# Performance work log

Measured on AMD Instinct MI355X. Metric: run time of the kernel, lower is better.

The kernel has to match this reference:

```python
import jax, jax.numpy as jnp
import numpy as np

STATE_DIM = 67  # latent_dim 64 + (x, y, yaw)
IU0, IU1 = np.triu_indices(STATE_DIM)  # row-major i<=j, matches nested loop order
DT = 0.1


def _conv_relu(x, w, b):
    # x: (B, Cin, L), w: (Cout, Cin, 5), stride 2, pad 2 -> (B, Cout, ceil(L/2))
    y = jax.lax.conv_general_dilated(x, w, window_strides=(2,), padding=[(2, 2)],
                                     dimension_numbers=('NCH', 'OIH', 'NCH'))
    return jax.nn.relu(y + b[None, :, None])


def setup_inputs() -> dict:
    key = jax.random.key(0)
    ks = jax.random.split(key, 13)
    B = 32768
    s = 0.05
    return {
        'lidar_in': jax.random.normal(ks[0], (B, 360), jnp.float32),
        'odom_in': jax.random.normal(ks[1], (B, 3), jnp.float32),
        'conv1_w': jax.random.normal(ks[2], (16, 1, 5), jnp.float32) * s,
        'conv1_b': jax.random.normal(ks[3], (16,), jnp.float32) * s,
        'conv2_w': jax.random.normal(ks[4], (32, 16, 5), jnp.float32) * s,
        'conv2_b': jax.random.normal(ks[5], (32,), jnp.float32) * s,
        'conv3_w': jax.random.normal(ks[6], (64, 32, 5), jnp.float32) * s,
        'conv3_b': jax.random.normal(ks[7], (64,), jnp.float32) * s,
        'fc_w': jax.random.normal(ks[8], (64, 64 * 45), jnp.float32) * 0.01,
        'fc_b': jax.random.normal(ks[9], (64,), jnp.float32) * s,
        'sindy_w': jax.random.normal(ks[10], (3, 2480), jnp.float32) * 0.01,
    }


def reference(lidar_in, odom_in, conv1_w, conv1_b, conv2_w, conv2_b,
              conv3_w, conv3_b, fc_w, fc_b, sindy_w):
    B = lidar_in.shape[0]
    # --- LiDAR feature extractor ---
    x = lidar_in[:, None, :]                       # (B, 1, 360)
    x = _conv_relu(x, conv1_w, conv1_b)            # (B, 16, 180)
    x = _conv_relu(x, conv2_w, conv2_b)            # (B, 32, 90)
    x = _conv_relu(x, conv3_w, conv3_b)            # (B, 64, 45)
    x = x.reshape(B, -1)                           # (B, 2880)
    z = x @ fc_w.T + fc_b                          # (B, 64)
    # --- state and SINDy library ---
    state = jnp.concatenate([z, odom_in], axis=1)  # (B, 67)
    quad = state[:, IU0] * state[:, IU1]           # (B, 2278) triangular products
    library = jnp.concatenate([
        jnp.ones((B, 1), state.dtype), state, quad,
        jnp.sin(state), jnp.cos(state)], axis=1)   # (B, 2480)
    dxyz = library @ sindy_w.T                     # (B, 3)
    return odom_in + DT * dxyz                     # (x,y,yaw)_next
```

## Files before the change

### kernel.cpp

```cpp
#include <hip/hip_runtime.h>
#include <hip/hip_bf16.h>

typedef __attribute__((ext_vector_type(8))) short bf16x8;
typedef __attribute__((ext_vector_type(4))) short short4v;
typedef __attribute__((ext_vector_type(4))) float f32x4;
typedef __attribute__((ext_vector_type(4))) float float4v;
typedef __attribute__((ext_vector_type(4))) int int4v;

constexpr int L0 = 360, L2n = 90, L3n = 45;
constexpr int SD = 67, NQ = 2278, LIB = 2480, FCIN = 2880;
constexpr int C1_CH = 20, S1B = 186 * C1_CH * 2;
constexpr int C2_CH = 44, S2B = 96 * C2_CH * 2;
constexpr int S3E = 2888;
constexpr int XB_STRIDE = 392;

constexpr int A_C3 = 0;
constexpr int A_C3SZ = 8 * S3E * 2;
constexpr int A_C1 = A_C3 + A_C3SZ;
constexpr int A_C1SZ = 2 * S1B;
constexpr int A_C2 = A_C1 + A_C1SZ;
constexpr int A_C2SZ = 2 * S2B + 512;
constexpr int A_XB = A_C2 + A_C2SZ;
constexpr int A_XBSZ = 2 * XB_STRIDE * 2;
constexpr int A_PAR = A_XB + A_XBSZ;
constexpr int A_SMEM = A_PAR + 448;
static_assert(A_SMEM <= 81920, "A LDS over 2-block budget");

constexpr int B_ST = 0;
constexpr int B_STSZ = 64 * 68 * 4;
constexpr int B_SB = B_ST + B_STSZ;
constexpr int B_SBSZ = 64 * 104 * 2;
constexpr int B_YB = B_SB + B_SBSZ;
constexpr int B_YBSZ = 3 * 64 * 84 * 2;
constexpr int B_SMEM = B_YB + B_YBSZ;
static_assert(B_SMEM <= 81920, "B LDS over 2-block budget");

constexpr size_t WSO_FCW = 0;
constexpr size_t WSO_W2F = WSO_FCW + 64 * FCIN * 2;
constexpr size_t WSO_W3F = WSO_W2F + 3 * 32 * 32 * 2;
constexpr size_t WSO_UB  = WSO_W3F + 5 * 64 * 32 * 2;
constexpr size_t WSO_W1F = WSO_UB + 3 * 80 * 96 * 2;
constexpr size_t WS_WEIGHTS = WSO_W1F + 16 * 32 * 2;
constexpr size_t WSO_C3 = WS_WEIGHTS;

__device__ __forceinline__ short f2b(float f) {
    return (short)__builtin_bit_cast(unsigned short, __float2bfloat16(f));
}
__device__ __forceinline__ float b2f(short s) {
    unsigned int u = ((unsigned int)(unsigned short)s) << 16;
    return __builtin_bit_cast(float, u);
}
__device__ __forceinline__ bf16x8 ld_frag8(const char* p) {
    union { bf16x8 v; short4v h[2]; } u;
    u.h[0] = *(const short4v*)(p);
    u.h[1] = *(const short4v*)(p + 8);
    return u.v;
}

__global__ __launch_bounds__(256) void pre_convert(
    const float* __restrict__ fcw, const float* __restrict__ w2,
    const float* __restrict__ w3, const float* __restrict__ w1,
    const float* __restrict__ sw, char* __restrict__ ws) {
    int idx = blockIdx.x * 256 + threadIdx.x;
    if (idx < 64 * FCIN) {
        int j = idx / FCIN, mp = idx % FCIN;
        int o = mp & 63, t = mp >> 6;
        ((short*)(ws + WSO_FCW))[idx] = f2b(fcw[j * FCIN + o * 45 + t]);
    }
    if (idx < 3 * 32 * 32) {
        int p = idx >> 10, o = (idx >> 5) & 31, k32 = idx & 31;
        int kk = 2 * p + (k32 >> 4), ic = k32 & 15;
        float v = (kk < 5) ? w2[(o * 16 + ic) * 5 + kk] : 0.f;
        ((short*)(ws + WSO_W2F))[idx] = f2b(v);
    }
    if (idx < 5 * 64 * 32) {
        int kk = idx >> 11, o = (idx >> 5) & 63, ic = idx & 31;
        ((short*)(ws + WSO_W3F))[idx] = f2b(w3[(o * 32 + ic) * 5 + kk]);
    }
    if (idx < 3 * 80 * 96) {
        int r = idx / (80 * 96), rem = idx % (80 * 96), nn = rem / 96, kk = rem % 96;
        float v = 0.f;
        if (nn < 68 && kk < 68) {
            if (nn == 67 && kk == 67) v = sw[r * LIB];
            else if (nn == 67) v = 0.5f * sw[r * LIB + 1 + kk];
            else if (kk == 67) v = 0.5f * sw[r * LIB + 1 + nn];
            else {
                int a = nn < kk ? nn : kk, b = nn < kk ? kk : nn;
                int q = a * 67 - (a * (a - 1)) / 2 + (b - a);
                v = sw[r * LIB + 68 + q];
                if (nn != kk) v *= 0.5f;
            }
        }
        ((short*)(ws + WSO_UB))[idx] = f2b(v);
    }
    if (idx < 512) {
        int o = idx >> 5, k = idx & 31;
        ((short*)(ws + WSO_W1F))[idx] = (k < 5) ? f2b(w1[o * 5 + k]) : (short)0;
    }
}

__global__ __launch_bounds__(512, 2) void conv_pipe(
    const float* __restrict__ lidar, const float* __restrict__ b1,
    const float* __restrict__ b2, const float* __restrict__ b3,
    char* __restrict__ ws)
{
    __shared__ char smem[A_SMEM];
    const int tid = threadIdx.x;
    const int wv = tid >> 6, lane = tid & 63;
    const int lr = lane & 15, lg = lane >> 4;
    const long blk = blockIdx.x;
    float* par = (float*)(smem + A_PAR);
    short* xb = (short*)(smem + A_XB);

    const int sW = wv & 1;
    const int qW = wv >> 1;
    const int o0_2 = (qW >> 1) * 16;
    const int o0_3 = qW * 16;

    bf16x8 af1 = *(const bf16x8*)(ws + WSO_W1F + (lr * 32 + lg * 8) * 2);
    bf16x8 af2[3], af3[5];
    #pragma unroll
    for (int p = 0; p < 3; p++)
        af2[p] = *(const bf16x8*)(ws + WSO_W2F + ((p * 32 + o0_2 + lr) * 32 + lg * 8) * 2);
    #pragma unroll
    for (int kk = 0; kk < 5; kk++)
        af3[kk] = *(const bf16x8*)(ws + WSO_W3F + ((kk * 64 + o0_3 + lr) * 32 + lg * 8) * 2);

    auto stage_xb = [&](int g) {
        float4v v = ((const float4v*)(lidar + (blk * 8 + g * 2) * L0))[tid];
        int si = tid / 90, c = tid % 90;
        short* dst = xb + si * XB_STRIDE + 2 + 4 * c;
        *(int*)(dst) = (int)(unsigned short)f2b(v[0]) | ((int)(unsigned short)f2b(v[1]) << 16);
        *(int*)(dst + 2) = (int)(unsigned short)f2b(v[2]) | ((int)(unsigned short)f2b(v[3]) << 16);
    };

    if (tid < 16) par[tid] = b1[tid];
    else if (tid < 48) par[16 + tid - 16] = b2[tid - 16];
    else if (tid < 112) par[48 + tid - 48] = b3[tid - 48];
    if (tid >= 120 && tid < 124) {
        int s = (tid - 120) >> 1, h = (tid - 120) & 1;
        ((int*)xb)[s * (XB_STRIDE / 2) + (h ? 181 : 0)] = 0;
    }
    if (tid >= 128 && tid < 208) {
        int i = tid - 128, slot = i / 40, r = i % 40;
        const int rows[4] = {2, 3, 184, 185};
        *(int*)(smem + A_C1 + slot * S1B + rows[r / 10] * (C1_CH * 2) + (r % 10) * 4) = 0;
    }
    if (tid >= 208 && tid < 384) {
        int i = tid - 208, slot = i / 88, r = i % 88;
        const int rows[4] = {2, 3, 94, 95};
        *(int*)(smem + A_C2 + slot * S2B + rows[r / 22] * (C2_CH * 2) + (r % 22) * 4) = 0;
    }
    if (tid < 180) stage_xb(0);
    __syncthreads();

    float bia1_[4], bia2_[4], bia3_[4];
    #pragma unroll
    for (int r = 0; r < 4; r++) {
        bia1_[r] = par[lg * 4 + r];
        bia2_[r] = par[16 + o0_2 + lg * 4 + r];
        bia3_[r] = par[48 + o0_3 + lg * 4 + r];
    }

    auto conv1_body = [&]() {
        const short* xs = xb + sW * XB_STRIDE;
        char* c1s = smem + A_C1 + sW * S1B;
        #pragma unroll
        for (int i = 0; i < 3; ++i) {
            const int t = (qW * 3 + i) * 16 + lr;
            bf16x8 bv = {0, 0, 0, 0, 0, 0, 0, 0};
            if (lg == 0) {
                const short* xp = xs + 2 * t;
                int d0 = *(const int*)(xp);
                int d1 = *(const int*)(xp + 2);
                bv[0] = (short)(d0 & 0xffff); bv[1] = (short)(d0 >> 16);
                bv[2] = (short)(d1 & 0xffff); bv[3] = (short)(d1 >> 16);
                bv[4] = xp[4];
            }
            f32x4 acc = {0.f, 0.f, 0.f, 0.f};
            acc = __builtin_amdgcn_mfma_f32_16x16x32_bf16(af1, bv, acc, 0, 0, 0);
            if (t < 180) {
                short4v pk = { f2b(fmaxf(acc[0] + bia1_[0], 0.f)), f2b(fmaxf(acc[1] + bia1_[1], 0.f)),
                               f2b(fmaxf(acc[2] + bia1_[2], 0.f)), f2b(fmaxf(acc[3] + bia1_[3], 0.f)) };
                *(short4v*)(c1s + (t + 4) * (C1_CH * 2) + lg * 8) = pk;
            }
        }
    };

    conv1_body();
    __syncthreads();

    for (int g = 0; g < 4; ++g) {
        {
            const int orow = o0_2 + lg * 4;
            const int kkp = lane >> 5, i0 = (lg & 1) * 8;
            const char* bp = smem + A_C1 + sW * S1B
                           + (2 * lr + kkp + 2) * (C1_CH * 2) + i0 * 2
                           + (qW & 1) * 3840;
            char* c2s = smem + A_C2 + sW * S2B;
            const bool stg = (g < 3) && (tid < 180);
            float4v lv;
            if (stg) lv = ((const float4v*)(lidar + (blk * 8 + (g + 1) * 2) * L0))[tid];
            #pragma unroll
            for (int i = 0; i < 3; ++i) {
                f32x4 acc = {0.f, 0.f, 0.f, 0.f};
                #pragma unroll
                for (int p = 0; p < 3; p++) {
                    bf16x8 bf = ld_frag8(bp + i * 1280 + p * 80);
                    acc = __builtin_amdgcn_mfma_f32_16x16x32_bf16(af2[p], bf, acc, 0, 0, 0);
                }
                const int tw = ((qW & 1) * 3 + i) * 16 + lr;
                if (tw < L2n) {
                    short4v pk = { f2b(fmaxf(acc[0] + bia2_[0], 0.f)), f2b(fmaxf(acc[1] + bia2_[1], 0.f)),
                                   f2b(fmaxf(acc[2] + bia2_[2], 0.f)), f2b(fmaxf(acc[3] + bia2_[3], 0.f)) };
                    *(short4v*)(c2s + (tw + 4) * (C2_CH * 2) + orow * 2) = pk;
                }
            }
            if (stg) {
                int si = tid / 90, c = tid % 90;
                short* dst = xb + si * XB_STRIDE + 2 + 4 * c;
                *(int*)(dst) = (int)(unsigned short)f2b(lv[0]) | ((int)(unsigned short)f2b(lv[1]) << 16);
                *(int*)(dst + 2) = (int)(unsigned short)f2b(lv[2]) | ((int)(unsigned short)f2b(lv[3]) << 16);
            }
        }
        __syncthreads();

        {
            const int orow = o0_3 + lg * 4;
            const char* bp2 = smem + A_C2 + sW * S2B
                            + (2 * lr + 2) * (C2_CH * 2) + lg * 16;
            char* c3s = smem + A_C3 + (g * 2 + sW) * (S3E * 2);
            #pragma unroll
            for (int tt = 0; tt < 3; ++tt) {
                f32x4 acc = {0.f, 0.f, 0.f, 0.f};
                #pragma unroll
                for (int kk = 0; kk < 5; kk++) {
                    bf16x8 bf = ld_frag8(bp2 + tt * 2816 + kk * 88);
                    acc = __builtin_amdgcn_mfma_f32_16x16x32_bf16(af3[kk], bf, acc, 0, 0, 0);
                }
                const int tw = tt * 16 + lr;
                if (tw < L3n) {
                    short4v pk = { f2b(fmaxf(acc[0] + bia3_[0], 0.f)), f2b(fmaxf(acc[1] + bia3_[1], 0.f)),
                                   f2b(fmaxf(acc[2] + bia3_[2], 0.f)), f2b(fmaxf(acc[3] + bia3_[3], 0.f)) };
                    int byteoff = (tw * 64 + orow) * 2;
                    byteoff ^= (tw & 7) << 4;
                    *(short4v*)(c3s + byteoff) = pk;
                }
            }
            if (g < 3) conv1_body();
        }
        __syncthreads();
    }

    for (int i4 = tid; i4 < 8 * 361; i4 += 512) {
        int k8 = i4 >> 3, sample = i4 & 7;
        int wb = k8 * 16;
        int src = wb ^ (((k8 >> 3) & 7) << 4);
        int4v v = *(const int4v*)(smem + A_C3 + sample * (S3E * 2) + src);
        ((int4v*)(ws + WSO_C3))[(blk * 361 + k8) * 8 + sample] = v;
    }
}

__global__ __launch_bounds__(512, 2) void fc_tail(
    const float* __restrict__ odom, const float* __restrict__ fcb,
    const float* __restrict__ sw, const char* __restrict__ ws,
    float* __restrict__ out)
{
    __shared__ char smem[B_SMEM];
    const int tid = threadIdx.x;
    const int wv = tid >> 6, lane = tid & 63;
    const int lr = lane & 15, lg = lane >> 4;
    const long blk = blockIdx.x;
    const long sbase = blk * 64;
    const short* c3g = (const short*)(ws + WSO_C3);
    const short* fcwb = (const short*)(ws + WSO_FCW);
    float* st = (float*)(smem + B_ST);
    short* sb = (short*)(smem + B_SB);
    short* yb = (short*)(smem + B_YB);

    {
        const int jt = wv & 3, mh = wv >> 2, j0 = jt * 16;
        const float fj = fcb[j0 + lr];
        const short* brow = fcwb + (long)(j0 + lr) * FCIN + lg * 8;
        const int sb0 = mh * 32;
        const long n0 = sbase + sb0 + lr;
        const long n1 = n0 + 16;
        const short* ar0 = c3g + ((n0 >> 3) * 361 + lg) * 64 + (n0 & 7) * 8;
        const short* ar1 = c3g + ((n1 >> 3) * 361 + lg) * 64 + (n1 & 7) * 8;
        f32x4 acc0 = {0.f, 0.f, 0.f, 0.f}, acc1 = {0.f, 0.f, 0.f, 0.f};
        bf16x8 a0 = *(const bf16x8*)(ar0);
        bf16x8 a1 = *(const bf16x8*)(ar1);
        bf16x8 b0 = *(const bf16x8*)(brow);
        for (int kt = 0; kt < 90; ++kt) {
            bf16x8 ac0 = a0, ac1 = a1, bc = b0;
            if (kt < 89) {
                a0 = *(const bf16x8*)(ar0 + (kt + 1) * 256);
                a1 = *(const bf16x8*)(ar1 + (kt + 1) * 256);
                b0 = *(const bf16x8*)(brow + (kt + 1) * 32);
            }
            acc0 = __builtin_amdgcn_mfma_f32_16x16x32_bf16(ac0, bc, acc0, 0, 0, 0);
            acc1 = __builtin_amdgcn_mfma_f32_16x16x32_bf16(ac1, bc, acc1, 0, 0, 0);
        }
        #pragma unroll
        for (int r = 0; r < 4; ++r) {
            st[(sb0 + lg * 4 + r) * 68 + j0 + lr] = acc0[r] + fj;
            st[(sb0 + 16 + lg * 4 + r) * 68 + j0 + lr] = acc1[r] + fj;
        }
    }
    __syncthreads();

    for (int i = tid; i < 64 * 104; i += 512) {
        int sr = i / 104, c = i % 104;
        short v;
        if (c < 64) v = f2b(st[sr * 68 + c]);
        else if (c < 67) v = f2b(odom[(sbase + sr) * 3 + (c - 64)]);
        else if (c == 67) v = (short)0x3F80;
        else v = 0;
        sb[i] = v;
    }
    __syncthreads();

    {
        const short* ubb = (const short*)(ws + WSO_UB);
        for (int job = wv; job < 15; job += 8) {
            const int r = job / 5, nt = job % 5;
            const short* ub = ubb + (r * 80 + nt * 16 + lr) * 96 + lg * 8;
            #pragma unroll
            for (int mt = 0; mt < 4; ++mt) {
                f32x4 acc = {0.f, 0.f, 0.f, 0.f};
                #pragma unroll
                for (int kt = 0; kt < 3; ++kt) {
                    bf16x8 av = *(const bf16x8*)(sb + (mt * 16 + lr) * 104 + kt * 32 + lg * 8);
                    bf16x8 bv = *(const bf16x8*)(ub + kt * 32);
                    acc = __builtin_amdgcn_mfma_f32_16x16x32_bf16(av, bv, acc, 0, 0, 0);
                }
                #pragma unroll
                for (int rr = 0; rr < 4; ++rr)
                    yb[(r * 64 + mt * 16 + lg * 4 + rr) * 84 + nt * 16 + lr] = f2b(acc[rr]);
            }
        }
    }
    __syncthreads();

    for (int ss = 0; ss < 8; ++ss) {
        const int sr = wv * 8 + ss;
        const long n = sbase + sr;
        float sv = st[sr * 68 + lane];
        float sn = __sinf(sv), cs = __cosf(sv);
        float d0 = sw[2346 + lane] * sn + sw[2413 + lane] * cs
                 + b2f(yb[(0 * 64 + sr) * 84 + lane]) * sv;
        float d1 = sw[LIB + 2346 + lane] * sn + sw[LIB + 2413 + lane] * cs
                 + b2f(yb[(1 * 64 + sr) * 84 + lane]) * sv;
        float d2 = sw[2 * LIB + 2346 + lane] * sn + sw[2 * LIB + 2413 + lane] * cs
                 + b2f(yb[(2 * 64 + sr) * 84 + lane]) * sv;
        if (lane < 3) {
            float ov = odom[n * 3 + lane];
            float sn2 = __sinf(ov), cs2 = __cosf(ov);
            int j2 = 64 + lane;
            d0 += sw[2346 + j2] * sn2 + sw[2413 + j2] * cs2 + b2f(yb[(0 * 64 + sr) * 84 + j2]) * ov;
            d1 += sw[LIB + 2346 + j2] * sn2 + sw[LIB + 2413 + j2] * cs2 + b2f(yb[(1 * 64 + sr) * 84 + j2]) * ov;
            d2 += sw[2 * LIB + 2346 + j2] * sn2 + sw[2 * LIB + 2413 + j2] * cs2 + b2f(yb[(2 * 64 + sr) * 84 + j2]) * ov;
        } else if (lane == 3) {
            d0 += b2f(yb[(0 * 64 + sr) * 84 + 67]);
            d1 += b2f(yb[(1 * 64 + sr) * 84 + 67]);
            d2 += b2f(yb[(2 * 64 + sr) * 84 + 67]);
        }
        #pragma unroll
        for (int off = 32; off; off >>= 1) {
            d0 += __shfl_xor(d0, off, 64);
            d1 += __shfl_xor(d1, off, 64);
            d2 += __shfl_xor(d2, off, 64);
        }
        if (lane == 0) {
            out[n * 3 + 0] = odom[n * 3 + 0] + 0.1f * d0;
            out[n * 3 + 1] = odom[n * 3 + 1] + 0.1f * d1;
            out[n * 3 + 2] = odom[n * 3 + 2] + 0.1f * d2;
        }
    }
}

extern "C" void kernel_launch(void* const* d_in, const int* in_sizes, int n_in,
                              void* d_out, int out_size, void* d_ws, size_t ws_size,
                              hipStream_t stream) {
    const float* lidar = (const float*)d_in[0];
    const float* odom  = (const float*)d_in[1];
    const float* w1    = (const float*)d_in[2];
    const float* b1    = (const float*)d_in[3];
    const float* w2    = (const float*)d_in[4];
    const float* b2    = (const float*)d_in[5];
    const float* w3    = (const float*)d_in[6];
    const float* b3    = (const float*)d_in[7];
    const float* fcw   = (const float*)d_in[8];
    const float* fcb   = (const float*)d_in[9];
    const float* sw    = (const float*)d_in[10];
    float* out = (float*)d_out;

    int B = in_sizes[0] / L0;
    size_t ws_total = WSO_C3 + (size_t)B * S3E * 2;
    if (ws_size < ws_total) return;

    char* ws = (char*)d_ws;
    pre_convert<<<(64 * FCIN + 255) / 256, 256, 0, stream>>>(fcw, w2, w3, w1, sw, ws);
    conv_pipe<<<B / 8, 512, 0, stream>>>(lidar, b1, b2, b3, ws);
    fc_tail<<<B / 64, 512, 0, stream>>>(odom, fcb, sw, ws, out);
}
```

Measured before the change: 194.7 us.

## Reuse conv2/conv3 B fragments across two output-channel tiles per wave

Conv2 and conv3 work is re-split so each wave computes two 16-channel output tiles sharing one loaded LDS B fragment, instead of one channel tile over three time tiles. This halves LDS fragment loads per MFMA and gives two independent accumulator chains. The time tiles are now split unevenly across waves (some waves do 2 tiles, others 1), which creates load imbalance. Holding twice as many weight fragments in registers also raises register pressure under the 512x2 launch bound.

```diff
diff --git a/kernel.cpp b/kernel.cpp
--- a/kernel.cpp
+++ b/kernel.cpp
@@ -114,17 +114,21 @@
 
     const int sW = wv & 1;
     const int qW = wv >> 1;
-    const int o0_2 = (qW >> 1) * 16;
-    const int o0_3 = qW * 16;
+    const int op3 = qW & 1;
+    const int th3 = qW >> 1;
 
     bf16x8 af1 = *(const bf16x8*)(ws + WSO_W1F + (lr * 32 + lg * 8) * 2);
-    bf16x8 af2[3], af3[5];
+    bf16x8 af2[2][3], af3[2][5];
     #pragma unroll
-    for (int p = 0; p < 3; p++)
-        af2[p] = *(const bf16x8*)(ws + WSO_W2F + ((p * 32 + o0_2 + lr) * 32 + lg * 8) * 2);
+    for (int ot = 0; ot < 2; ot++)
+        #pragma unroll
+        for (int p = 0; p < 3; p++)
+            af2[ot][p] = *(const bf16x8*)(ws + WSO_W2F + ((p * 32 + ot * 16 + lr) * 32 + lg * 8) * 2);
     #pragma unroll
-    for (int kk = 0; kk < 5; kk++)
-        af3[kk] = *(const bf16x8*)(ws + WSO_W3F + ((kk * 64 + o0_3 + lr) * 32 + lg * 8) * 2);
+    for (int j = 0; j < 2; j++)
+        #pragma unroll
+        for (int kk = 0; kk < 5; kk++)
+            af3[j][kk] = *(const bf16x8*)(ws + WSO_W3F + ((kk * 64 + (op3 * 2 + j) * 16 + lr) * 32 + lg * 8) * 2);
 
     auto stage_xb = [&](int g) {
         float4v v = ((const float4v*)(lidar + (blk * 8 + g * 2) * L0))[tid];
@@ -154,12 +158,14 @@
     if (tid < 180) stage_xb(0);
     __syncthreads();
 
-    float bia1_[4], bia2_[4], bia3_[4];
+    float bia1_[4], bia2_[2][4], bia3_[2][4];
     #pragma unroll
     for (int r = 0; r < 4; r++) {
         bia1_[r] = par[lg * 4 + r];
-        bia2_[r] = par[16 + o0_2 + lg * 4 + r];
-        bia3_[r] = par[48 + o0_3 + lg * 4 + r];
+        #pragma unroll
+        for (int ot = 0; ot < 2; ot++) bia2_[ot][r] = par[16 + ot * 16 + lg * 4 + r];
+        #pragma unroll
+        for (int j = 0; j < 2; j++) bia3_[j][r] = par[48 + (op3 * 2 + j) * 16 + lg * 4 + r];
     }
 
     auto conv1_body = [&]() {
@@ -192,28 +198,34 @@
 
     for (int g = 0; g < 4; ++g) {
         {
-            const int orow = o0_2 + lg * 4;
             const int kkp = lane >> 5, i0 = (lg & 1) * 8;
             const char* bp = smem + A_C1 + sW * S1B
-                           + (2 * lr + kkp + 2) * (C1_CH * 2) + i0 * 2
-                           + (qW & 1) * 3840;
+                           + (2 * lr + kkp + 2) * (C1_CH * 2) + i0 * 2;
             char* c2s = smem + A_C2 + sW * S2B;
             const bool stg = (g < 3) && (tid < 180);
             float4v lv;
             if (stg) lv = ((const float4v*)(lidar + (blk * 8 + (g + 1) * 2) * L0))[tid];
-            #pragma unroll
-            for (int i = 0; i < 3; ++i) {
-                f32x4 acc = {0.f, 0.f, 0.f, 0.f};
+
+            const int tbase = (qW < 2) ? qW * 2 : (2 + qW);
+            const int nT = (qW < 2) ? 2 : 1;
+            for (int it = 0; it < nT; ++it) {
+                const int T = tbase + it;
+                f32x4 a0 = {0.f, 0.f, 0.f, 0.f}, a1 = {0.f, 0.f, 0.f, 0.f};
                 #pragma unroll
                 for (int p = 0; p < 3; p++) {
-                    bf16x8 bf = ld_frag8(bp + i * 1280 + p * 80);
-                    acc = __builtin_amdgcn_mfma_f32_16x16x32_bf16(af2[p], bf, acc, 0, 0, 0);
+                    bf16x8 bf = ld_frag8(bp + T * 1280 + p * 80);
+                    a0 = __builtin_amdgcn_mfma_f32_16x16x32_bf16(af2[0][p], bf, a0, 0, 0, 0);
+                    a1 = __builtin_amdgcn_mfma_f32_16x16x32_bf16(af2[1][p], bf, a1, 0, 0, 0);
                 }
-                const int tw = ((qW & 1) * 3 + i) * 16 + lr;
+                const int tw = T * 16 + lr;
                 if (tw < L2n) {
-                    short4v pk = { f2b(fmaxf(acc[0] + bia2_[0], 0.f)), f2b(fmaxf(acc[1] + bia2_[1], 0.f)),
-                                   f2b(fmaxf(acc[2] + bia2_[2], 0.f)), f2b(fmaxf(acc[3] + bia2_[3], 0.f)) };
-                    *(short4v*)(c2s + (tw + 4) * (C2_CH * 2) + orow * 2) = pk;
+                    short4v pk0 = { f2b(fmaxf(a0[0] + bia2_[0][0], 0.f)), f2b(fmaxf(a0[1] + bia2_[0][1], 0.f)),
+                                    f2b(fmaxf(a0[2] + bia2_[0][2], 0.f)), f2b(fmaxf(a0[3] + bia2_[0][3], 0.f)) };
+                    short4v pk1 = { f2b(fmaxf(a1[0] + bia2_[1][0], 0.f)), f2b(fmaxf(a1[1] + bia2_[1][1], 0.f)),
+                                    f2b(fmaxf(a1[2] + bia2_[1][2], 0.f)), f2b(fmaxf(a1[3] + bia2_[1][3], 0.f)) };
+                    char* wp = c2s + (tw + 4) * (C2_CH * 2);
+                    *(short4v*)(wp + lg * 8) = pk0;
+                    *(short4v*)(wp + 32 + lg * 8) = pk1;
                 }
             }
             if (stg) {
@@ -226,25 +238,32 @@
         __syncthreads();
 
         {
-            const int orow = o0_3 + lg * 4;
             const char* bp2 = smem + A_C2 + sW * S2B
                             + (2 * lr + 2) * (C2_CH * 2) + lg * 16;
             char* c3s = smem + A_C3 + (g * 2 + sW) * (S3E * 2);
-            #pragma unroll
-            for (int tt = 0; tt < 3; ++tt) {
-                f32x4 acc = {0.f, 0.f, 0.f, 0.f};
+            const int ttbase = (th3 == 0) ? 0 : 2;
+            const int nT3 = (th3 == 0) ? 2 : 1;
+            for (int it = 0; it < nT3; ++it) {
+                const int tt = ttbase + it;
+                f32x4 a0 = {0.f, 0.f, 0.f, 0.f}, a1 = {0.f, 0.f, 0.f, 0.f};
                 #pragma unroll
                 for (int kk = 0; kk < 5; kk++) {
                     bf16x8 bf = ld_frag8(bp2 + tt * 2816 + kk * 88);
-                    acc = __builtin_amdgcn_mfma_f32_16x16x32_bf16(af3[kk], bf, acc, 0, 0, 0);
+                    a0 = __builtin_amdgcn_mfma_f32_16x16x32_bf16(af3[0][kk], bf, a0, 0, 0, 0);
+                    a1 = __builtin_amdgcn_mfma_f32_16x16x32_bf16(af3[1][kk], bf, a1, 0, 0, 0);
                 }
                 const int tw = tt * 16 + lr;
                 if (tw < L3n) {
-                    short4v pk = { f2b(fmaxf(acc[0] + bia3_[0], 0.f)), f2b(fmaxf(acc[1] + bia3_[1], 0.f)),
-                                   f2b(fmaxf(acc[2] + bia3_[2], 0.f)), f2b(fmaxf(acc[3] + bia3_[3], 0.f)) };
-                    int byteoff = (tw * 64 + orow) * 2;
-                    byteoff ^= (tw & 7) << 4;
-                    *(short4v*)(c3s + byteoff) = pk;
+                    short4v pk0 = { f2b(fmaxf(a0[0] + bia3_[0][0], 0.f)), f2b(fmaxf(a0[1] + bia3_[0][1], 0.f)),
+                                    f2b(fmaxf(a0[2] + bia3_[0][2], 0.f)), f2b(fmaxf(a0[3] + bia3_[0][3], 0.f)) };
+                    short4v pk1 = { f2b(fmaxf(a1[0] + bia3_[1][0], 0.f)), f2b(fmaxf(a1[1] + bia3_[1][1], 0.f)),
+                                    f2b(fmaxf(a1[2] + bia3_[1][2], 0.f)), f2b(fmaxf(a1[3] + bia3_[1][3], 0.f)) };
+                    const int orow0 = op3 * 32 + lg * 4;
+                    const int orow1 = op3 * 32 + 16 + lg * 4;
+                    int bo0 = ((tw * 64 + orow0) * 2) ^ ((tw & 7) << 4);
+                    int bo1 = ((tw * 64 + orow1) * 2) ^ ((tw & 7) << 4);
+                    *(short4v*)(c3s + bo0) = pk0;
+                    *(short4v*)(c3s + bo1) = pk1;
                 }
             }
             if (g < 3) conv1_body();
```

New measurement: 241.2 us. 1.24x slower.
